# Optimization experiments

Hardware: AMD Instinct MI355X
Metric: run time of the kernel (lower is better)

## Reference

```python
import jax, jax.numpy as jnp
import numpy as np

D = 256        # node/edge feature dim
H = 256        # MLP hidden dim
NG = 80000     # grid (src) nodes
NM = 20000     # mesh (dst) nodes
E = 160000     # g2m edges
EPS = 1e-5


def _mlp(x, W1, b1, W2, b2, g, beta):
    # MeshGraphMLP with hidden_layers=1: Linear -> SiLU -> Linear -> LayerNorm
    h = jax.nn.silu(x @ W1 + b1)
    y = h @ W2 + b2
    mu = jnp.mean(y, axis=-1, keepdims=True)
    var = jnp.var(y, axis=-1, keepdims=True)
    return (y - mu) * jax.lax.rsqrt(var + EPS) * g + beta


def setup_inputs() -> dict:
    key = jax.random.key(0)
    ks = jax.random.split(key, 16)

    def rn(k, shape, s=0.02):
        return jax.random.normal(k, shape, dtype=jnp.float32) * s

    inp = {
        "g2m_efeat": jax.random.normal(ks[0], (E, D), dtype=jnp.float32),
        "grid_nfeat": jax.random.normal(ks[1], (NG, D), dtype=jnp.float32),
        "mesh_nfeat": jax.random.normal(ks[2], (NM, D), dtype=jnp.float32),
        "src_idx": jax.random.randint(ks[3], (E,), 0, NG, dtype=jnp.int32),
        "dst_idx": jax.random.randint(ks[4], (E,), 0, NM, dtype=jnp.int32),
        # edge MLP (concat variant): input = [efeat | src_feat | dst_feat] -> 3D
        "eW1": rn(ks[5], (3 * D, H)), "eb1": jnp.zeros((H,), jnp.float32),
        "eW2": rn(ks[6], (H, D)),     "eb2": jnp.zeros((D,), jnp.float32),
        "eg": jnp.ones((D,), jnp.float32), "ebeta": jnp.zeros((D,), jnp.float32),
        # src node MLP: D -> H -> D
        "sW1": rn(ks[7], (D, H)), "sb1": jnp.zeros((H,), jnp.float32),
        "sW2": rn(ks[8], (H, D)), "sb2": jnp.zeros((D,), jnp.float32),
        "sg": jnp.ones((D,), jnp.float32), "sbeta": jnp.zeros((D,), jnp.float32),
        # dst node MLP: (D_agg + D_node) = 2D -> H -> D
        "dW1": rn(ks[9], (2 * D, H)), "db1": jnp.zeros((H,), jnp.float32),
        "dW2": rn(ks[10], (H, D)),    "db2": jnp.zeros((D,), jnp.float32),
        "dg": jnp.ones((D,), jnp.float32), "dbeta": jnp.zeros((D,), jnp.float32),
    }
    return inp


def reference(g2m_efeat, grid_nfeat, mesh_nfeat, src_idx, dst_idx,
              eW1, eb1, eW2, eb2, eg, ebeta,
              sW1, sb1, sW2, sb2, sg, sbeta,
              dW1, db1, dW2, db2, dg, dbeta):
    # edge MLP: gather src/dst node features, concat with edge features
    e_in = jnp.concatenate(
        [g2m_efeat, grid_nfeat[src_idx], mesh_nfeat[dst_idx]], axis=-1)  # [E, 3D]
    efeat = _mlp(e_in, eW1, eb1, eW2, eb2, eg, ebeta)                    # [E, D]
    # aggregate_and_concat: copy_e_sum scatter to dst mesh nodes, concat node feats
    agg = jax.ops.segment_sum(efeat, dst_idx, num_segments=NM)           # [NM, D]
    cat_feat = jnp.concatenate([agg, mesh_nfeat], axis=-1)               # [NM, 2D]
    mesh_out = mesh_nfeat + _mlp(cat_feat, dW1, db1, dW2, db2, dg, dbeta)
    grid_out = grid_nfeat + _mlp(grid_nfeat, sW1, sb1, sW2, sb2, sg, sbeta)
    return (grid_out, mesh_out)
```

## Files before the change

kernel.cpp:

```cpp
#include <hip/hip_runtime.h>
#include <hip/hip_bf16.h>

#define DD 256
#define NGN 80000
#define NMN 20000
#define NEE 160000

typedef unsigned short u16;
typedef __attribute__((ext_vector_type(8))) short s16x8;
typedef __attribute__((ext_vector_type(4))) short s16x4;
typedef __attribute__((ext_vector_type(4))) float f32x4;

__device__ __forceinline__ u16 f2bf(float f) {
  __hip_bfloat16 h = __float2bfloat16(f);
  union { __hip_bfloat16 h; u16 u; } v; v.h = h;
  return v.u;
}
__device__ __forceinline__ float bf2f(u16 x) {
  union { unsigned u; float f; } v; v.u = ((unsigned)x) << 16;
  return v.f;
}
__device__ __forceinline__ float silu(float x) {
  return x * __builtin_amdgcn_rcpf(1.f + __expf(-x));
}

__device__ __forceinline__ void gload16(const void* g, void* l) {
  __builtin_amdgcn_global_load_lds(
      (const __attribute__((address_space(1))) void*)g,
      (__attribute__((address_space(3))) void*)l, 16, 0, 0);
}

__device__ __forceinline__ s16x8 ldsA(const u16* uni, int rowL, int cL) {
  int swz = (rowL & 7) << 4;
  s16x4 lo = *(const s16x4*)((const char*)uni + rowL * 512 + ((cL * 2) ^ swz));
  s16x4 hi = *(const s16x4*)((const char*)uni + rowL * 512 + (((cL + 16) * 2) ^ swz));
  s16x8 a;
#pragma unroll
  for (int j = 0; j < 4; ++j) { a[j] = lo[j]; a[4 + j] = hi[j]; }
  return a;
}

__global__ void pack_hist(const float* __restrict__ eW1, const float* __restrict__ eW2,
                          const float* __restrict__ sW1, const float* __restrict__ sW2,
                          const float* __restrict__ dW1, const float* __restrict__ dW2,
                          u16* __restrict__ wp, const int* __restrict__ didx,
                          int* __restrict__ cnt) {
  int bid = blockIdx.x;
  if (bid < 2304) {
    const float* W; u16* dst; int lb;
    if (bid < 768)       { W = eW1; dst = wp;              lb = bid; }
    else if (bid < 1024) { W = eW2; dst = wp + 768 * 256;  lb = bid - 768; }
    else if (bid < 1280) { W = sW1; dst = wp + 1024 * 256; lb = bid - 1024; }
    else if (bid < 1536) { W = sW2; dst = wp + 1280 * 256; lb = bid - 1280; }
    else if (bid < 2048) { W = dW1; dst = wp + 1536 * 256; lb = bid - 1536; }
    else                 { W = dW2; dst = wp + 2048 * 256; lb = bid - 2048; }
    int idx = lb * 256 + threadIdx.x;
    int i = idx & 7, lane = (idx >> 3) & 63, nt = (idx >> 9) & 15, kt = idx >> 13;
    int k = kt * 32 + 4 * (lane >> 4) + (i < 4 ? i : 12 + i);
    int n = nt * 16 + (lane & 15);
    dst[idx] = f2bf(W[(size_t)k * 256 + n]);
  } else {
    int i = (bid - 2304) * 256 + threadIdx.x;
    if (i < NEE) atomicAdd(cnt + didx[i], 1);
  }
}

__global__ void csr_scan(const int* __restrict__ cnt, int* __restrict__ cursor) {
  __shared__ int psum[256];
  const int CH = (NMN + 255) / 256;
  int t = threadIdx.x;
  int base = t * CH, s = 0;
  for (int k = 0; k < CH; ++k) { int i = base + k; if (i < NMN) s += cnt[i]; }
  psum[t] = s;
  __syncthreads();
  for (int off = 1; off < 256; off <<= 1) {
    int v = (t >= off) ? psum[t - off] : 0;
    __syncthreads();
    psum[t] += v;
    __syncthreads();
  }
  int run = psum[t] - s;
  for (int k = 0; k < CH; ++k) {
    int i = base + k;
    if (i < NMN) { cursor[i] = run; run += cnt[i]; }
  }
}

__device__ __forceinline__ void gemm_body(char* lds, const float* __restrict__ X,
                                          const u16* __restrict__ Wp, u16* __restrict__ Y,
                                          int n, int blk) {
  const int tid = threadIdx.x;
  const int lane = tid & 63;
  const int wave = tid >> 6;
  const int mr = wave >> 1, nc = wave & 1;
  const int g = lane >> 4, lr = lane & 15;
  const int row0 = blk * 64;

#pragma unroll
  for (int t = 0; t < 16; ++t) {
    int e = wave * 16 + t;
    int r = min(row0 + e, n - 1);
    const float* gsrc = X + (size_t)r * DD + ((((lane * 16) ^ ((e & 7) << 4))) >> 2);
    gload16(gsrc, lds + e * 1024);
  }
  __syncthreads();

  const f32x4 fz = {0.f, 0.f, 0.f, 0.f};
  f32x4 acc[2][8];
#pragma unroll
  for (int mt = 0; mt < 2; ++mt)
#pragma unroll
    for (int nt = 0; nt < 8; ++nt) acc[mt][nt] = fz;

  for (int kl = 0; kl < 8; ++kl) {
    s16x8 afr[2];
#pragma unroll
    for (int mt = 0; mt < 2; ++mt) {
      int row = mr * 32 + mt * 16 + lr;
      int sw = (row & 7) << 4;
      const char* bse = lds + row * 1024;
      f32x4 lo = *(const f32x4*)(bse + ((kl * 128 + g * 16) ^ sw));
      f32x4 hi = *(const f32x4*)(bse + ((kl * 128 + g * 16 + 64) ^ sw));
      s16x8 a;
#pragma unroll
      for (int j = 0; j < 4; ++j) { a[j] = (short)f2bf(lo[j]); a[4 + j] = (short)f2bf(hi[j]); }
      afr[mt] = a;
    }
#pragma unroll
    for (int h = 0; h < 2; ++h) {
      s16x8 bfr[4];
#pragma unroll
      for (int q = 0; q < 4; ++q)
        bfr[q] = *(const s16x8*)(Wp + (size_t)kl * 8192 + ((nc * 8 + h * 4 + q) * 64 + lane) * 8);
#pragma unroll
      for (int q = 0; q < 4; ++q) {
        acc[0][h * 4 + q] = __builtin_amdgcn_mfma_f32_16x16x32_bf16(afr[0], bfr[q], acc[0][h * 4 + q], 0, 0, 0);
        acc[1][h * 4 + q] = __builtin_amdgcn_mfma_f32_16x16x32_bf16(afr[1], bfr[q], acc[1][h * 4 + q], 0, 0, 0);
      }
    }
  }
  __syncthreads();
  u16* uni = (u16*)lds;
#pragma unroll
  for (int mt = 0; mt < 2; ++mt)
#pragma unroll
    for (int nt = 0; nt < 8; ++nt)
#pragma unroll
      for (int i = 0; i < 4; ++i) {
        int rowL = mr * 32 + mt * 16 + 4 * g + i;
        int col = nc * 128 + nt * 16 + lr;
        *(u16*)((char*)uni + rowL * 512 + ((col * 2) ^ ((rowL & 7) << 4))) = f2bf(acc[mt][nt][i]);
      }
  __syncthreads();
#pragma unroll
  for (int rr = 0; rr < 16; ++rr) {
    int rowL = wave * 16 + rr;
    int rg = row0 + rowL;
    if (rg < n) {
      s16x4 v = *(const s16x4*)((char*)uni + rowL * 512 + ((lane * 8) ^ ((rowL & 7) << 4)));
      *(s16x4*)(Y + (size_t)rg * DD + lane * 4) = v;
    }
  }
}

template <int MODE, int K1>
__device__ __forceinline__ void mlp_body(
    u16* uni, float2 (*pstats)[2],
    const float* __restrict__ xa, const float* __restrict__ xb,
    const u16* __restrict__ W1p, const float* __restrict__ b1,
    const u16* __restrict__ W2p, const float* __restrict__ b2,
    const float* __restrict__ gam, const float* __restrict__ bet,
    const float* __restrict__ resid, float* __restrict__ out, int nrows, int blk) {
  const int tid = threadIdx.x;
  const int lane = tid & 63;
  const int wave = tid >> 6;
  const int mr = wave >> 1, nc = wave & 1;
  const int g = lane >> 4, lr = lane & 15;
  const int row0 = blk * 64;

  const f32x4 fz = {0.f, 0.f, 0.f, 0.f};
  f32x4 acc[2][8];
#pragma unroll
  for (int mt = 0; mt < 2; ++mt)
#pragma unroll
    for (int nt = 0; nt < 8; ++nt) acc[mt][nt] = fz;

#pragma unroll
  for (int region = 0; region < K1 / 256; ++region) {
    __syncthreads();
    const float* Xr = (region == 0) ? xa : xb;
#pragma unroll
    for (int j = 0; j < 8; ++j) {
      int e = wave * 16 + j * 2 + (lane >> 5);
      int r = min(row0 + e, nrows - 1);
      const float* src = Xr + (size_t)r * DD + (lane & 31) * 8;
      f32x4 f0 = *(const f32x4*)src;
      f32x4 f1 = *(const f32x4*)(src + 4);
      s16x8 o;
#pragma unroll
      for (int k = 0; k < 4; ++k) { o[k] = (short)f2bf(f0[k]); o[4 + k] = (short)f2bf(f1[k]); }
      int co = (lane & 31) * 8;
      *(s16x8*)((char*)uni + e * 512 + ((co * 2) ^ ((e & 7) << 4))) = o;
    }
    __syncthreads();
    for (int kl = 0; kl < 8; ++kl) {
      const int kt = region * 8 + kl;
      s16x8 afr[2];
#pragma unroll
      for (int mt = 0; mt < 2; ++mt) afr[mt] = ldsA(uni, mr * 32 + mt * 16 + lr, kl * 32 + 4 * g);
#pragma unroll
      for (int h = 0; h < 2; ++h) {
        s16x8 bfr[4];
#pragma unroll
        for (int q = 0; q < 4; ++q)
          bfr[q] = *(const s16x8*)(W1p + (size_t)kt * 8192 + ((nc * 8 + h * 4 + q) * 64 + lane) * 8);
#pragma unroll
        for (int q = 0; q < 4; ++q) {
          acc[0][h * 4 + q] = __builtin_amdgcn_mfma_f32_16x16x32_bf16(afr[0], bfr[q], acc[0][h * 4 + q], 0, 0, 0);
          acc[1][h * 4 + q] = __builtin_amdgcn_mfma_f32_16x16x32_bf16(afr[1], bfr[q], acc[1][h * 4 + q], 0, 0, 0);
        }
      }
    }
  }
  __syncthreads();

  {
    float b1v[8];
#pragma unroll
    for (int nt = 0; nt < 8; ++nt) b1v[nt] = b1[nc * 128 + nt * 16 + lr];
#pragma unroll
    for (int mt = 0; mt < 2; ++mt)
#pragma unroll
      for (int nt = 0; nt < 8; ++nt)
#pragma unroll
        for (int i = 0; i < 4; ++i) {
          float x = acc[mt][nt][i] + b1v[nt];
          float h = silu(x);
          int rowL = mr * 32 + mt * 16 + 4 * g + i;
          int col = nc * 128 + nt * 16 + lr;
          *(u16*)((char*)uni + rowL * 512 + ((col * 2) ^ ((rowL & 7) << 4))) = f2bf(h);
        }
  }
  __syncthreads();

#pragma unroll
  for (int mt = 0; mt < 2; ++mt)
#pragma unroll
    for (int nt = 0; nt < 8; ++nt) acc[mt][nt] = fz;
  for (int kl = 0; kl < 8; ++kl) {
    s16x8 afr[2];
#pragma unroll
    for (int mt = 0; mt < 2; ++mt) afr[mt] = ldsA(uni, mr * 32 + mt * 16 + lr, kl * 32 + 4 * g);
#pragma unroll
    for (int h = 0; h < 2; ++h) {
      s16x8 bfr[4];
#pragma unroll
      for (int q = 0; q < 4; ++q)
        bfr[q] = *(const s16x8*)(W2p + (size_t)kl * 8192 + ((nc * 8 + h * 4 + q) * 64 + lane) * 8);
#pragma unroll
      for (int q = 0; q < 4; ++q) {
        acc[0][h * 4 + q] = __builtin_amdgcn_mfma_f32_16x16x32_bf16(afr[0], bfr[q], acc[0][h * 4 + q], 0, 0, 0);
        acc[1][h * 4 + q] = __builtin_amdgcn_mfma_f32_16x16x32_bf16(afr[1], bfr[q], acc[1][h * 4 + q], 0, 0, 0);
      }
    }
  }

  float b2v[8], gv[8], bv[8];
#pragma unroll
  for (int nt = 0; nt < 8; ++nt) {
    int col = nc * 128 + nt * 16 + lr;
    b2v[nt] = b2[col];
    gv[nt] = gam[col];
    bv[nt] = bet[col];
  }
#pragma unroll
  for (int mt = 0; mt < 2; ++mt)
#pragma unroll
    for (int i = 0; i < 4; ++i) {
      float s = 0.f, s2 = 0.f;
#pragma unroll
      for (int nt = 0; nt < 8; ++nt) {
        float y = acc[mt][nt][i] + b2v[nt];
        s += y;
        s2 += y * y;
      }
#pragma unroll
      for (int m = 1; m < 16; m <<= 1) {
        s += __shfl_xor(s, m);
        s2 += __shfl_xor(s2, m);
      }
      if (lr == 0) pstats[mr * 32 + mt * 16 + 4 * g + i][nc] = make_float2(s, s2);
    }
  __syncthreads();
#pragma unroll
  for (int mt = 0; mt < 2; ++mt)
#pragma unroll
    for (int i = 0; i < 4; ++i) {
      int rowL = mr * 32 + mt * 16 + 4 * g + i;
      float2 pa = pstats[rowL][0], pb = pstats[rowL][1];
      float sum = pa.x + pb.x, sq = pa.y + pb.y;
      float mu = sum * (1.f / 256.f);
      float var = fmaxf(sq * (1.f / 256.f) - mu * mu, 0.f);
      float rs = rsqrtf(var + 1e-5f);
      int rg = row0 + rowL;
      if (MODE == 2 && rg >= nrows) continue;
#pragma unroll
      for (int nt = 0; nt < 8; ++nt) {
        int col = nc * 128 + nt * 16 + lr;
        float y = acc[mt][nt][i] + b2v[nt];
        float val = (y - mu) * rs * gv[nt] + bv[nt];
        out[(size_t)rg * DD + col] = resid[(size_t)rg * DD + col] + val;
      }
    }
}

__global__ __launch_bounds__(256, 2) void gemm_fill(
    const float* __restrict__ efeat, const float* __restrict__ gridf,
    const float* __restrict__ mesh, const u16* __restrict__ wp,
    u16* __restrict__ ECp, u16* __restrict__ GSp, u16* __restrict__ GMp,
    const int* __restrict__ didx, int* __restrict__ cursor, int* __restrict__ eids,
    const float* __restrict__ sb1, const float* __restrict__ sb2,
    const float* __restrict__ sg, const float* __restrict__ sbt,
    float* __restrict__ gout, int withMlp) {
  __shared__ char ldsblob[65536];
  __shared__ float2 pstats[64][2];
  int bid = blockIdx.x;
  if (withMlp) {
    if (bid < 3750) {
      if ((bid % 3) == 2) {
        mlp_body<1, 256>((u16*)ldsblob, pstats, gridf, nullptr, wp + 1024 * 256, sb1,
                         wp + 1280 * 256, sb2, sg, sbt, gridf, gout, NGN, bid / 3);
        return;
      }
      gemm_body(ldsblob, efeat, wp, ECp, NEE, (bid / 3) * 2 + (bid % 3));
      return;
    }
    bid -= 1250;
  }
  if (bid < 2500) gemm_body(ldsblob, efeat, wp, ECp, NEE, bid);
  else if (bid < 3750) gemm_body(ldsblob, gridf, wp + 8 * 8192, GSp, NGN, bid - 2500);
  else if (bid < 4063) gemm_body(ldsblob, mesh, wp + 16 * 8192, GMp, NMN, bid - 3750);
  else {
    int e = (bid - 4063) * 256 + threadIdx.x;
    if (e < NEE) { int p = atomicAdd(cursor + didx[e], 1); eids[p] = e; }
  }
}

__global__ __launch_bounds__(256, 3) void edge_kern(
    const u16* __restrict__ ECp, const u16* __restrict__ GSp, const u16* __restrict__ GMp,
    const int* __restrict__ sidx, const int* __restrict__ eids,
    const float* __restrict__ b1,
    const u16* __restrict__ W2p, const float* __restrict__ b2,
    const float* __restrict__ gam, const float* __restrict__ bet,
    const int* __restrict__ didx, float* __restrict__ agg) {
  __shared__ u16 uni[16384];
  __shared__ float2 pstats[64][2];
  __shared__ int eidL[64], srcL[64], dstL[64];

  const int tid = threadIdx.x;
  const int lane = tid & 63;
  const int wave = tid >> 6;
  const int mr = wave >> 1, nc = wave & 1;
  const int g = lane >> 4, lr = lane & 15;
  const int row0 = blockIdx.x * 64;

  if (tid < 64) {
    int e = eids[row0 + tid];
    eidL[tid] = e;
    srcL[tid] = sidx[e];
    dstL[tid] = didx[e];
  }
  __syncthreads();

  const int co = (lane & 31) * 8;
  f32x4 b1a = *(const f32x4*)(b1 + co);
  f32x4 b1b = *(const f32x4*)(b1 + co + 4);
#pragma unroll
  for (int j = 0; j < 8; ++j) {
    int e = wave * 16 + j * 2 + (lane >> 5);
    s16x8 va = *(const s16x8*)(ECp + (size_t)eidL[e] * DD + co);
    s16x8 vb = *(const s16x8*)(GSp + (size_t)srcL[e] * DD + co);
    s16x8 vc = *(const s16x8*)(GMp + (size_t)dstL[e] * DD + co);
    s16x8 o;
#pragma unroll
    for (int k = 0; k < 8; ++k) {
      float bk = (k < 4) ? b1a[k] : b1b[k - 4];
      float x = bf2f((u16)va[k]) + bf2f((u16)vb[k]) + bf2f((u16)vc[k]) + bk;
      o[k] = (short)f2bf(silu(x));
    }
    *(s16x8*)((char*)uni + e * 512 + ((co * 2) ^ ((e & 7) << 4))) = o;
  }
  __syncthreads();

  const f32x4 fz = {0.f, 0.f, 0.f, 0.f};
  f32x4 acc[2][8];
#pragma unroll
  for (int mt = 0; mt < 2; ++mt)
#pragma unroll
    for (int nt = 0; nt < 8; ++nt) acc[mt][nt] = fz;
  for (int kl = 0; kl < 8; ++kl) {
    s16x8 afr[2];
#pragma unroll
    for (int mt = 0; mt < 2; ++mt) afr[mt] = ldsA(uni, mr * 32 + mt * 16 + lr, kl * 32 + 4 * g);
#pragma unroll
    for (int h = 0; h < 2; ++h) {
      s16x8 bfr[4];
#pragma unroll
      for (int q = 0; q < 4; ++q)
        bfr[q] = *(const s16x8*)(W2p + (size_t)kl * 8192 + ((nc * 8 + h * 4 + q) * 64 + lane) * 8);
#pragma unroll
      for (int q = 0; q < 4; ++q) {
        acc[0][h * 4 + q] = __builtin_amdgcn_mfma_f32_16x16x32_bf16(afr[0], bfr[q], acc[0][h * 4 + q], 0, 0, 0);
        acc[1][h * 4 + q] = __builtin_amdgcn_mfma_f32_16x16x32_bf16(afr[1], bfr[q], acc[1][h * 4 + q], 0, 0, 0);
      }
    }
  }

  float b2v[8], gv[8], bv[8];
#pragma unroll
  for (int nt = 0; nt < 8; ++nt) {
    int col = nc * 128 + nt * 16 + lr;
    b2v[nt] = b2[col];
    gv[nt] = gam[col];
    bv[nt] = bet[col];
  }
#pragma unroll
  for (int mt = 0; mt < 2; ++mt)
#pragma unroll
    for (int i = 0; i < 4; ++i) {
      float s = 0.f, s2 = 0.f;
#pragma unroll
      for (int nt = 0; nt < 8; ++nt) {
        float y = acc[mt][nt][i] + b2v[nt];
        s += y;
        s2 += y * y;
      }
#pragma unroll
      for (int m = 1; m < 16; m <<= 1) {
        s += __shfl_xor(s, m);
        s2 += __shfl_xor(s2, m);
      }
      if (lr == 0) pstats[mr * 32 + mt * 16 + 4 * g + i][nc] = make_float2(s, s2);
    }
  __syncthreads();

#pragma unroll
  for (int mt = 0; mt < 2; ++mt)
#pragma unroll
    for (int i = 0; i < 4; ++i) {
      int rowL = mr * 32 + mt * 16 + 4 * g + i;
      float2 pa = pstats[rowL][0], pb = pstats[rowL][1];
      float sum = pa.x + pb.x, sq = pa.y + pb.y;
      float mu = sum * (1.f / 256.f);
      float var = fmaxf(sq * (1.f / 256.f) - mu * mu, 0.f);
      float rs = rsqrtf(var + 1e-5f);
#pragma unroll
      for (int nt = 0; nt < 8; ++nt) {
        int col = nc * 128 + nt * 16 + lr;
        float y = acc[mt][nt][i] + b2v[nt];
        float val = (y - mu) * rs * gv[nt] + bv[nt];
        *(u16*)((char*)uni + rowL * 512 + ((col * 2) ^ ((rowL & 7) << 4))) = f2bf(val);
      }
    }
  __syncthreads();

  {
    int c = tid;
    float sum = 0.f;
    int prev = dstL[0];
#pragma unroll 8
    for (int r = 0; r < 64; ++r) {
      int d = dstL[r];
      if (d != prev) {
        atomicAdd(agg + (size_t)prev * DD + c, sum);
        sum = 0.f;
        prev = d;
      }
      sum += bf2f(*(const u16*)((char*)uni + r * 512 + ((c * 2) ^ ((r & 7) << 4))));
    }
    atomicAdd(agg + (size_t)prev * DD + c, sum);
  }
}

__global__ __launch_bounds__(256, 3) void mlp12_kernel(
    const float* __restrict__ agg, const float* __restrict__ mesh,
    const u16* __restrict__ dW1p, const float* __restrict__ db1,
    const u16* __restrict__ dW2p, const float* __restrict__ db2,
    const float* __restrict__ dg, const float* __restrict__ dbt,
    float* __restrict__ mout,
    const float* __restrict__ gridf,
    const u16* __restrict__ sW1p, const float* __restrict__ sb1,
    const u16* __restrict__ sW2p, const float* __restrict__ sb2,
    const float* __restrict__ sg, const float* __restrict__ sbt,
    float* __restrict__ gout, int withMlp1) {
  __shared__ u16 uni[16384];
  __shared__ float2 pstats[64][2];
  int bid = blockIdx.x;
  if (bid < 313) {
    mlp_body<2, 512>(uni, pstats, agg, mesh, dW1p, db1, dW2p, db2, dg, dbt,
                     mesh, mout, NMN, bid);
  } else if (withMlp1) {
    mlp_body<1, 256>(uni, pstats, gridf, nullptr, sW1p, sb1, sW2p, sb2,
                     sg, sbt, gridf, gout, NGN, bid - 313);
  }
}

extern "C" void kernel_launch(void* const* d_in, const int* in_sizes, int n_in,
                              void* d_out, int out_size, void* d_ws, size_t ws_size,
                              hipStream_t stream) {
  const float* g2m  = (const float*)d_in[0];
  const float* grid = (const float*)d_in[1];
  const float* mesh = (const float*)d_in[2];
  const int* sidx = (const int*)d_in[3];
  const int* didx = (const int*)d_in[4];
  const float* eW1 = (const float*)d_in[5];
  const float* eb1 = (const float*)d_in[6];
  const float* eW2 = (const float*)d_in[7];
  const float* eb2 = (const float*)d_in[8];
  const float* eg  = (const float*)d_in[9];
  const float* ebt = (const float*)d_in[10];
  const float* sW1 = (const float*)d_in[11];
  const float* sb1 = (const float*)d_in[12];
  const float* sW2 = (const float*)d_in[13];
  const float* sb2 = (const float*)d_in[14];
  const float* sg  = (const float*)d_in[15];
  const float* sbt = (const float*)d_in[16];
  const float* dW1 = (const float*)d_in[17];
  const float* db1 = (const float*)d_in[18];
  const float* dW2 = (const float*)d_in[19];
  const float* db2 = (const float*)d_in[20];
  const float* dg  = (const float*)d_in[21];
  const float* dbt = (const float*)d_in[22];

  char* w = (char*)d_ws;
  float* agg = (float*)w;
  u16* wp = (u16*)(w + 20480000);
  int* cnt = (int*)(w + 20480000 + 1179648);
  int* cursor = cnt + 20480;
  int* eids = cursor + 20480;
  const size_t GS_OFF = 22463488;
  const size_t EC_OFF = GS_OFF + (size_t)NGN * DD * 2 + (size_t)NMN * DD * 2;
  const size_t NEED_BIG = EC_OFF + (size_t)NEE * DD * 2;

  u16* eW1p = wp;
  u16* eW2p = eW1p + 768 * 256;
  u16* sW1p = eW2p + 256 * 256;
  u16* sW2p = sW1p + 256 * 256;
  u16* dW1p = sW2p + 256 * 256;
  u16* dW2p = dW1p + 512 * 256;

  float* gout = (float*)d_out;
  float* mout = gout + (size_t)NGN * DD;

  u16* GSp = (u16*)(w + GS_OFF);
  u16* GMp = GSp + (size_t)NGN * DD;
  const bool big = ws_size >= NEED_BIG;
  u16* ECp = big ? (u16*)(w + EC_OFF) : (u16*)d_out;

  (void)hipMemsetAsync(agg, 0, 20480000, stream);
  (void)hipMemsetAsync(cnt, 0, 81920, stream);

  pack_hist<<<2304 + 625, 256, 0, stream>>>(eW1, eW2, sW1, sW2, dW1, dW2, wp, didx, cnt);
  csr_scan<<<1, 256, 0, stream>>>(cnt, cursor);

  if (big) {
    gemm_fill<<<5938, 256, 0, stream>>>(g2m, grid, mesh, wp, ECp, GSp, GMp,
                                        didx, cursor, eids,
                                        sb1, sb2, sg, sbt, gout, 1);
    edge_kern<<<2500, 256, 0, stream>>>(
        ECp, GSp, GMp, sidx, eids, eb1, eW2p, eb2, eg, ebt, didx, agg);
    mlp12_kernel<<<313, 256, 0, stream>>>(
        agg, mesh, dW1p, db1, dW2p, db2, dg, dbt, mout,
        grid, sW1p, sb1, sW2p, sb2, sg, sbt, gout, 0);
  } else {
    gemm_fill<<<4688, 256, 0, stream>>>(g2m, grid, mesh, wp, ECp, GSp, GMp,
                                        didx, cursor, eids,
                                        sb1, sb2, sg, sbt, gout, 0);
    edge_kern<<<2500, 256, 0, stream>>>(
        ECp, GSp, GMp, sidx, eids, eb1, eW2p, eb2, eg, ebt, didx, agg);
    mlp12_kernel<<<313 + 1250, 256, 0, stream>>>(
        agg, mesh, dW1p, db1, dW2p, db2, dg, dbt, mout,
        grid, sW1p, sb1, sW2p, sb2, sg, sbt, gout, 1);
  }
}
```

Before: 393.0 us.

## Halve GEMM row tile to 32 and raise gemm_fill occupancy

The pre-projection GEMM body now handles 32 rows per block instead of 64, which halves LDS use to 32KB and lets gemm_fill use launch bounds of 3 blocks per CU. Grid sizes and block-index mappings are recomputed to match. In edge_kern, all gathered rows are loaded into registers before any compute so the gather loads can be in flight together, and the hidden activations move to a separate LDS buffer. Several k-loops get an unroll-2 pragma. Smaller tiles mean B-fragment weights are reloaded per 16-row tile rather than shared across two, which raises weight traffic per output row.

```diff
diff --git a/kernel.cpp b/kernel.cpp
--- a/kernel.cpp
+++ b/kernel.cpp
@@ -86,19 +86,19 @@
   }
 }
 
-__device__ __forceinline__ void gemm_body(char* lds, const float* __restrict__ X,
-                                          const u16* __restrict__ Wp, u16* __restrict__ Y,
-                                          int n, int blk) {
+__device__ __forceinline__ void gemm_body32(char* lds, const float* __restrict__ X,
+                                            const u16* __restrict__ Wp, u16* __restrict__ Y,
+                                            int n, int blk) {
   const int tid = threadIdx.x;
   const int lane = tid & 63;
   const int wave = tid >> 6;
   const int mr = wave >> 1, nc = wave & 1;
   const int g = lane >> 4, lr = lane & 15;
-  const int row0 = blk * 64;
-
-#pragma unroll
-  for (int t = 0; t < 16; ++t) {
-    int e = wave * 16 + t;
+  const int row0 = blk * 32;
+
+#pragma unroll
+  for (int t = 0; t < 8; ++t) {
+    int e = wave * 8 + t;
     int r = min(row0 + e, n - 1);
     const float* gsrc = X + (size_t)r * DD + ((((lane * 16) ^ ((e & 7) << 4))) >> 2);
     gload16(gsrc, lds + e * 1024);
@@ -106,26 +106,20 @@
   __syncthreads();
 
   const f32x4 fz = {0.f, 0.f, 0.f, 0.f};
-  f32x4 acc[2][8];
-#pragma unroll
-  for (int mt = 0; mt < 2; ++mt)
-#pragma unroll
-    for (int nt = 0; nt < 8; ++nt) acc[mt][nt] = fz;
-
+  f32x4 acc[8];
+#pragma unroll
+  for (int nt = 0; nt < 8; ++nt) acc[nt] = fz;
+
+#pragma unroll 2
   for (int kl = 0; kl < 8; ++kl) {
-    s16x8 afr[2];
-#pragma unroll
-    for (int mt = 0; mt < 2; ++mt) {
-      int row = mr * 32 + mt * 16 + lr;
-      int sw = (row & 7) << 4;
-      const char* bse = lds + row * 1024;
-      f32x4 lo = *(const f32x4*)(bse + ((kl * 128 + g * 16) ^ sw));
-      f32x4 hi = *(const f32x4*)(bse + ((kl * 128 + g * 16 + 64) ^ sw));
-      s16x8 a;
-#pragma unroll
-      for (int j = 0; j < 4; ++j) { a[j] = (short)f2bf(lo[j]); a[4 + j] = (short)f2bf(hi[j]); }
-      afr[mt] = a;
-    }
+    int row = mr * 16 + lr;
+    int sw = (row & 7) << 4;
+    const char* bse = lds + row * 1024;
+    f32x4 lo = *(const f32x4*)(bse + ((kl * 128 + g * 16) ^ sw));
+    f32x4 hi = *(const f32x4*)(bse + ((kl * 128 + g * 16 + 64) ^ sw));
+    s16x8 afr;
+#pragma unroll
+    for (int j = 0; j < 4; ++j) { afr[j] = (short)f2bf(lo[j]); afr[4 + j] = (short)f2bf(hi[j]); }
 #pragma unroll
     for (int h = 0; h < 2; ++h) {
       s16x8 bfr[4];
@@ -133,28 +127,24 @@
       for (int q = 0; q < 4; ++q)
         bfr[q] = *(const s16x8*)(Wp + (size_t)kl * 8192 + ((nc * 8 + h * 4 + q) * 64 + lane) * 8);
 #pragma unroll
-      for (int q = 0; q < 4; ++q) {
-        acc[0][h * 4 + q] = __builtin_amdgcn_mfma_f32_16x16x32_bf16(afr[0], bfr[q], acc[0][h * 4 + q], 0, 0, 0);
-        acc[1][h * 4 + q] = __builtin_amdgcn_mfma_f32_16x16x32_bf16(afr[1], bfr[q], acc[1][h * 4 + q], 0, 0, 0);
-      }
+      for (int q = 0; q < 4; ++q)
+        acc[h * 4 + q] = __builtin_amdgcn_mfma_f32_16x16x32_bf16(afr, bfr[q], acc[h * 4 + q], 0, 0, 0);
     }
   }
   __syncthreads();
   u16* uni = (u16*)lds;
 #pragma unroll
-  for (int mt = 0; mt < 2; ++mt)
-#pragma unroll
-    for (int nt = 0; nt < 8; ++nt)
-#pragma unroll
-      for (int i = 0; i < 4; ++i) {
-        int rowL = mr * 32 + mt * 16 + 4 * g + i;
-        int col = nc * 128 + nt * 16 + lr;
-        *(u16*)((char*)uni + rowL * 512 + ((col * 2) ^ ((rowL & 7) << 4))) = f2bf(acc[mt][nt][i]);
-      }
-  __syncthreads();
-#pragma unroll
-  for (int rr = 0; rr < 16; ++rr) {
-    int rowL = wave * 16 + rr;
+  for (int nt = 0; nt < 8; ++nt)
+#pragma unroll
+    for (int i = 0; i < 4; ++i) {
+      int rowL = mr * 16 + 4 * g + i;
+      int col = nc * 128 + nt * 16 + lr;
+      *(u16*)((char*)uni + rowL * 512 + ((col * 2) ^ ((rowL & 7) << 4))) = f2bf(acc[nt][i]);
+    }
+  __syncthreads();
+#pragma unroll
+  for (int rr = 0; rr < 8; ++rr) {
+    int rowL = wave * 8 + rr;
     int rg = row0 + rowL;
     if (rg < n) {
       s16x4 v = *(const s16x4*)((char*)uni + rowL * 512 + ((lane * 8) ^ ((rowL & 7) << 4)));
@@ -203,6 +193,7 @@
       *(s16x8*)((char*)uni + e * 512 + ((co * 2) ^ ((e & 7) << 4))) = o;
     }
     __syncthreads();
+#pragma unroll 2
     for (int kl = 0; kl < 8; ++kl) {
       const int kt = region * 8 + kl;
       s16x8 afr[2];
@@ -247,6 +238,7 @@
   for (int mt = 0; mt < 2; ++mt)
 #pragma unroll
     for (int nt = 0; nt < 8; ++nt) acc[mt][nt] = fz;
+#pragma unroll 2
   for (int kl = 0; kl < 8; ++kl) {
     s16x8 afr[2];
 #pragma unroll
@@ -314,7 +306,7 @@
     }
 }
 
-__global__ __launch_bounds__(256, 2) void gemm_fill(
+__global__ __launch_bounds__(256, 3) void gemm_fill(
     const float* __restrict__ efeat, const float* __restrict__ gridf,
     const float* __restrict__ mesh, const u16* __restrict__ wp,
     u16* __restrict__ ECp, u16* __restrict__ GSp, u16* __restrict__ GMp,
@@ -322,26 +314,26 @@
     const float* __restrict__ sb1, const float* __restrict__ sb2,
     const float* __restrict__ sg, const float* __restrict__ sbt,
     float* __restrict__ gout, int withMlp) {
-  __shared__ char ldsblob[65536];
+  __shared__ char ldsblob[32768];
   __shared__ float2 pstats[64][2];
   int bid = blockIdx.x;
   if (withMlp) {
-    if (bid < 3750) {
-      if ((bid % 3) == 2) {
+    if (bid < 6250) {
+      if ((bid % 5) == 4) {
         mlp_body<1, 256>((u16*)ldsblob, pstats, gridf, nullptr, wp + 1024 * 256, sb1,
-                         wp + 1280 * 256, sb2, sg, sbt, gridf, gout, NGN, bid / 3);
+                         wp + 1280 * 256, sb2, sg, sbt, gridf, gout, NGN, bid / 5);
         return;
       }
-      gemm_body(ldsblob, efeat, wp, ECp, NEE, (bid / 3) * 2 + (bid % 3));
+      gemm_body32(ldsblob, efeat, wp, ECp, NEE, (bid / 5) * 4 + (bid % 5));
       return;
     }
     bid -= 1250;
   }
-  if (bid < 2500) gemm_body(ldsblob, efeat, wp, ECp, NEE, bid);
-  else if (bid < 3750) gemm_body(ldsblob, gridf, wp + 8 * 8192, GSp, NGN, bid - 2500);
-  else if (bid < 4063) gemm_body(ldsblob, mesh, wp + 16 * 8192, GMp, NMN, bid - 3750);
+  if (bid < 5000) gemm_body32(ldsblob, efeat, wp, ECp, NEE, bid);
+  else if (bid < 7500) gemm_body32(ldsblob, gridf, wp + 8 * 8192, GSp, NGN, bid - 5000);
+  else if (bid < 8125) gemm_body32(ldsblob, mesh, wp + 16 * 8192, GMp, NMN, bid - 7500);
   else {
-    int e = (bid - 4063) * 256 + threadIdx.x;
+    int e = (bid - 8125) * 256 + threadIdx.x;
     if (e < NEE) { int p = atomicAdd(cursor + didx[e], 1); eids[p] = e; }
   }
 }
@@ -353,7 +345,7 @@
     const u16* __restrict__ W2p, const float* __restrict__ b2,
     const float* __restrict__ gam, const float* __restrict__ bet,
     const int* __restrict__ didx, float* __restrict__ agg) {
-  __shared__ u16 uni[16384];
+  __shared__ u16 uni[8192];
   __shared__ float2 pstats[64][2];
   __shared__ int eidL[64], srcL[64], dstL[64];
 
@@ -375,20 +367,26 @@
   const int co = (lane & 31) * 8;
   f32x4 b1a = *(const f32x4*)(b1 + co);
   f32x4 b1b = *(const f32x4*)(b1 + co + 4);
+  s16x8 va[8], vb[8], vc[8];
 #pragma unroll
   for (int j = 0; j < 8; ++j) {
     int e = wave * 16 + j * 2 + (lane >> 5);
-    s16x8 va = *(const s16x8*)(ECp + (size_t)eidL[e] * DD + co);
-    s16x8 vb = *(const s16x8*)(GSp + (size_t)srcL[e] * DD + co);
-    s16x8 vc = *(const s16x8*)(GMp + (size_t)dstL[e] * DD + co);
+    va[j] = *(const s16x8*)(ECp + (size_t)eidL[e] * DD + co);
+    vb[j] = *(const s16x8*)(GSp + (size_t)srcL[e] * DD + co);
+    vc[j] = *(const s16x8*)(GMp + (size_t)dstL[e] * DD + co);
+  }
+  __shared__ u16 hbuf[16384];
+#pragma unroll
+  for (int j = 0; j < 8; ++j) {
+    int e = wave * 16 + j * 2 + (lane >> 5);
     s16x8 o;
 #pragma unroll
     for (int k = 0; k < 8; ++k) {
       float bk = (k < 4) ? b1a[k] : b1b[k - 4];
-      float x = bf2f((u16)va[k]) + bf2f((u16)vb[k]) + bf2f((u16)vc[k]) + bk;
+      float x = bf2f((u16)va[j][k]) + bf2f((u16)vb[j][k]) + bf2f((u16)vc[j][k]) + bk;
       o[k] = (short)f2bf(silu(x));
     }
-    *(s16x8*)((char*)uni + e * 512 + ((co * 2) ^ ((e & 7) << 4))) = o;
+    *(s16x8*)((char*)hbuf + e * 512 + ((co * 2) ^ ((e & 7) << 4))) = o;
   }
   __syncthreads();
 
@@ -398,10 +396,11 @@
   for (int mt = 0; mt < 2; ++mt)
 #pragma unroll
     for (int nt = 0; nt < 8; ++nt) acc[mt][nt] = fz;
+#pragma unroll 2
   for (int kl = 0; kl < 8; ++kl) {
     s16x8 afr[2];
 #pragma unroll
-    for (int mt = 0; mt < 2; ++mt) afr[mt] = ldsA(uni, mr * 32 + mt * 16 + lr, kl * 32 + 4 * g);
+    for (int mt = 0; mt < 2; ++mt) afr[mt] = ldsA(hbuf, mr * 32 + mt * 16 + lr, kl * 32 + 4 * g);
 #pragma unroll
     for (int h = 0; h < 2; ++h) {
       s16x8 bfr[4];
@@ -459,7 +458,7 @@
         int col = nc * 128 + nt * 16 + lr;
         float y = acc[mt][nt][i] + b2v[nt];
         float val = (y - mu) * rs * gv[nt] + bv[nt];
-        *(u16*)((char*)uni + rowL * 512 + ((col * 2) ^ ((rowL & 7) << 4))) = f2bf(val);
+        *(u16*)((char*)hbuf + rowL * 512 + ((col * 2) ^ ((rowL & 7) << 4))) = f2bf(val);
       }
     }
   __syncthreads();
@@ -476,7 +475,7 @@
         sum = 0.f;
         prev = d;
       }
-      sum += bf2f(*(const u16*)((char*)uni + r * 512 + ((c * 2) ^ ((r & 7) << 4))));
+      sum += bf2f(*(const u16*)((char*)hbuf + r * 512 + ((c * 2) ^ ((r & 7) << 4))));
     }
     atomicAdd(agg + (size_t)prev * DD + c, sum);
   }
@@ -564,16 +563,16 @@
   csr_scan<<<1, 256, 0, stream>>>(cnt, cursor);
 
   if (big) {
-    gemm_fill<<<5938, 256, 0, stream>>>(g2m, grid, mesh, wp, ECp, GSp, GMp,
-                                        didx, cursor, eids,
-                                        sb1, sb2, sg, sbt, gout, 1);
+    gemm_fill<<<10000, 256, 0, stream>>>(g2m, grid, mesh, wp, ECp, GSp, GMp,
+                                         didx, cursor, eids,
+                                         sb1, sb2, sg, sbt, gout, 1);
     edge_kern<<<2500, 256, 0, stream>>>(
         ECp, GSp, GMp, sidx, eids, eb1, eW2p, eb2, eg, ebt, didx, agg);
     mlp12_kernel<<<313, 256, 0, stream>>>(
         agg, mesh, dW1p, db1, dW2p, db2, dg, dbt, mout,
         grid, sW1p, sb1, sW2p, sb2, sg, sbt, gout, 0);
   } else {
-    gemm_fill<<<4688, 256, 0, stream>>>(g2m, grid, mesh, wp, ECp, GSp, GMp,
+    gemm_fill<<<8750, 256, 0, stream>>>(g2m, grid, mesh, wp, ECp, GSp, GMp,
                                         didx, cursor, eids,
                                         sb1, sb2, sg, sbt, gout, 0);
     edge_kern<<<2500, 256, 0, stream>>>(
```

Result: faster. 380.5 us (-3.2%).
